# Kernel tuning notes

Measured on AMD Instinct MI355X. Metric: run time of the kernel, lower is better.

Reference implementation:

```python
import jax, jax.numpy as jnp
import numpy as np
from math import sqrt

N_HEADS = 16

def setup_inputs() -> dict:
    key = jax.random.key(0)
    ks = jax.random.split(key, 6)
    B, T, C = 4, 2048, 1024
    s = 0.02
    return {
        "X": jax.random.normal(ks[0], (B, T, C), jnp.float32),
        "Wq": jax.random.normal(ks[1], (C, C), jnp.float32) * s,
        "Wk": jax.random.normal(ks[2], (C, C), jnp.float32) * s,
        "Wv": jax.random.normal(ks[3], (C, C), jnp.float32) * s,
        "Wo": jax.random.normal(ks[4], (C, C), jnp.float32) * s,
        "bo": jnp.zeros((C,), jnp.float32),
    }

def reference(X, Wq, Wk, Wv, Wo, bo):
    B, T, C = X.shape
    H = N_HEADS
    D = C // H
    scale = sqrt(C / H)  # == sqrt(D)
    # Linear layers (torch Linear: y = x @ W.T), split into heads: [B,H,T,D]
    Q = (X @ Wq.T).reshape(B, T, H, D).transpose(0, 2, 1, 3)
    K = (X @ Wk.T).reshape(B, T, H, D).transpose(0, 2, 1, 3)
    V = (X @ Wv.T).reshape(B, T, H, D).transpose(0, 2, 1, 3)
    A = jnp.einsum("bhtd,bhsd->bhts", Q, K) / scale  # [B,H,T,T]
    causal = jnp.tril(jnp.ones((T, T), dtype=bool))
    A = jnp.where(causal, A, -jnp.inf)
    A = jax.nn.softmax(A, axis=-1)
    Y = jnp.einsum("bhts,bhsd->bhtd", A, V)  # [B,H,T,D]
    Y = Y.transpose(0, 2, 1, 3).reshape(B, T, C)
    return Y @ Wo.T + bo
```

## Files before the change

### kernel.cpp

```cpp
#include <hip/hip_runtime.h>
#include <hip/hip_bf16.h>
#include <stdint.h>


typedef unsigned short u16;
typedef __attribute__((ext_vector_type(8))) __bf16 bf16x8;
typedef __attribute__((ext_vector_type(4))) float  f32x4;
typedef __attribute__((ext_vector_type(4))) unsigned short u16x4;
typedef __attribute__((ext_vector_type(8))) unsigned short u16x8;
typedef __attribute__((ext_vector_type(4))) short s16x4;

#define B_  4
#define T_  2048
#define C_  1024
#define H_  16
#define D_  64
#define BT_ (B_ * T_)

#define Q_SCALE 0.1803368801111204f

__device__ __forceinline__ u16 f32_to_bf16(float f) {
    unsigned int u = __float_as_uint(f);
    unsigned int r = (u + 0x7FFFu + ((u >> 16) & 1u)) >> 16;
    return (u16)r;
}

__device__ __forceinline__ unsigned int pk_bf16(float a, float b) {
    float2 f2; f2.x = a; f2.y = b;
    __hip_bfloat162 h = __float22bfloat162_rn(f2);
    return *(unsigned int*)&h;
}

__device__ __forceinline__ void async16(const void* g, void* lds) {
    __builtin_amdgcn_global_load_lds(
        (const __attribute__((address_space(1))) void*)g,
        (__attribute__((address_space(3))) void*)lds, 16, 0, 0);
}

__global__ void cast_bf16_kernel(const float* __restrict__ in, u16* __restrict__ out, int n4) {
    int i = blockIdx.x * 256 + threadIdx.x;
    if (i >= n4) return;
    float4 v = ((const float4*)in)[i];
    u16x4 o;
    o[0] = f32_to_bf16(v.x); o[1] = f32_to_bf16(v.y);
    o[2] = f32_to_bf16(v.z); o[3] = f32_to_bf16(v.w);
    ((u16x4*)out)[i] = o;
}

__global__ void cast_w4_kernel(const float* __restrict__ w0, const float* __restrict__ w1,
                               const float* __restrict__ w2, const float* __restrict__ w3,
                               u16* __restrict__ o0, u16* __restrict__ o1,
                               u16* __restrict__ o2, u16* __restrict__ o3) {
    int which = blockIdx.y;
    const float* in = (which == 0) ? w0 : (which == 1) ? w1 : (which == 2) ? w2 : w3;
    u16* out = (which == 0) ? o0 : (which == 1) ? o1 : (which == 2) ? o2 : o3;
    int i = blockIdx.x * 256 + threadIdx.x;
    float4 v = ((const float4*)in)[i];
    u16x4 o;
    o[0] = f32_to_bf16(v.x); o[1] = f32_to_bf16(v.y);
    o[2] = f32_to_bf16(v.z); o[3] = f32_to_bf16(v.w);
    ((u16x4*)out)[i] = o;
}

__global__ __launch_bounds__(256, 2) void qkv_gemm(
    const u16* __restrict__ Xb,
    const u16* __restrict__ Wqb, const u16* __restrict__ Wkb, const u16* __restrict__ Wvb,
    u16* __restrict__ Qb, u16* __restrict__ Kb, u16* __restrict__ Vtb)
{
    __shared__ u16 Xs[8192];
    __shared__ u16 Wqs[8192], Wks[8192], Wvs[8192];

    int id = blockIdx.x;
    int xcd = id & 7;
    int local = id >> 3;
    int tt = xcd * 8 + (local & 7);
    int ct = local >> 3;
    int m0 = tt * 128, n0 = ct * 128;

    int tid = threadIdx.x, lane = tid & 63, w = tid >> 6;
    int quad = lane >> 4, l15 = lane & 15;
    int wm = w >> 1, wn = w & 1;

    int c0 = tid, c1 = tid + 256;
    int row0 = c0 >> 2, row1 = c1 >> 2;
    int gc0 = (((c0 & 3) - (row0 >> 1)) & 3) * 8;
    int gc1 = (((c1 & 3) - (row1 >> 1)) & 3) * 8;
    int ldsb0 = (w * 64) * 16;
    int ldsb1 = (256 + w * 64) * 16;

    const u16* xp0 = Xb  + (size_t)(m0 + row0) * C_ + gc0;
    const u16* xp1 = Xb  + (size_t)(m0 + row1) * C_ + gc1;
    const u16* wq0 = Wqb + (size_t)(n0 + row0) * C_ + gc0;
    const u16* wq1 = Wqb + (size_t)(n0 + row1) * C_ + gc1;
    const u16* wk0 = Wkb + (size_t)(n0 + row0) * C_ + gc0;
    const u16* wk1 = Wkb + (size_t)(n0 + row1) * C_ + gc1;
    const u16* wv0 = Wvb + (size_t)(n0 + row0) * C_ + gc0;
    const u16* wv1 = Wvb + (size_t)(n0 + row1) * C_ + gc1;

    int aoff[4], boff[4];
#pragma unroll
    for (int i = 0; i < 4; ++i) {
        int rA = wm * 64 + i * 16 + l15;
        aoff[i] = (rA * 32 + (((rA >> 1) + quad) & 3) * 8) * 2;
        int rB = wn * 64 + i * 16 + l15;
        boff[i] = (rB * 32 + (((rB >> 1) + quad) & 3) * 8) * 2;
    }

    f32x4 aq[4][4], ak[4][4], av[4][4];
    const f32x4 z4 = {0.f, 0.f, 0.f, 0.f};
#pragma unroll
    for (int i = 0; i < 4; ++i)
#pragma unroll
        for (int j = 0; j < 4; ++j) { aq[i][j] = z4; ak[i][j] = z4; av[i][j] = z4; }

    async16(xp0, (char*)Xs  + ldsb0); async16(xp1, (char*)Xs  + ldsb1);
    async16(wq0, (char*)Wqs + ldsb0); async16(wq1, (char*)Wqs + ldsb1);
    async16(wk0, (char*)Wks + ldsb0); async16(wk1, (char*)Wks + ldsb1);
    async16(wv0, (char*)Wvs + ldsb0); async16(wv1, (char*)Wvs + ldsb1);
    xp0 += 32; xp1 += 32; wq0 += 32; wq1 += 32;
    wk0 += 32; wk1 += 32; wv0 += 32; wv1 += 32;

    auto body = [&](int kt, int cur, int nxt) {
        __syncthreads();
        if (kt + 1 < 32) {
            async16(xp0, (char*)Xs  + nxt + ldsb0); async16(xp1, (char*)Xs  + nxt + ldsb1);
            async16(wq0, (char*)Wqs + nxt + ldsb0); async16(wq1, (char*)Wqs + nxt + ldsb1);
            async16(wk0, (char*)Wks + nxt + ldsb0); async16(wk1, (char*)Wks + nxt + ldsb1);
            async16(wv0, (char*)Wvs + nxt + ldsb0); async16(wv1, (char*)Wvs + nxt + ldsb1);
        }
        xp0 += 32; xp1 += 32; wq0 += 32; wq1 += 32;
        wk0 += 32; wk1 += 32; wv0 += 32; wv1 += 32;

        bf16x8 xa[4];
#pragma unroll
        for (int i = 0; i < 4; ++i)
            xa[i] = *(const bf16x8*)((const char*)Xs + cur + aoff[i]);

        bf16x8 bb[4];
#pragma unroll
        for (int j = 0; j < 4; ++j)
            bb[j] = *(const bf16x8*)((const char*)Wqs + cur + boff[j]);
#pragma unroll
        for (int j = 0; j < 4; ++j)
#pragma unroll
            for (int i = 0; i < 4; ++i)
                aq[j][i] = __builtin_amdgcn_mfma_f32_16x16x32_bf16(bb[j], xa[i], aq[j][i], 0, 0, 0);

#pragma unroll
        for (int j = 0; j < 4; ++j)
            bb[j] = *(const bf16x8*)((const char*)Wks + cur + boff[j]);
#pragma unroll
        for (int j = 0; j < 4; ++j)
#pragma unroll
            for (int i = 0; i < 4; ++i)
                ak[j][i] = __builtin_amdgcn_mfma_f32_16x16x32_bf16(bb[j], xa[i], ak[j][i], 0, 0, 0);

#pragma unroll
        for (int j = 0; j < 4; ++j)
            bb[j] = *(const bf16x8*)((const char*)Wvs + cur + boff[j]);
#pragma unroll
        for (int i = 0; i < 4; ++i)
#pragma unroll
            for (int j = 0; j < 4; ++j)
                av[i][j] = __builtin_amdgcn_mfma_f32_16x16x32_bf16(xa[i], bb[j], av[i][j], 0, 0, 0);
    };

    for (int kt = 0; kt < 32; kt += 2) {
        body(kt,     0,    8192);
        body(kt + 1, 8192, 0);
    }

#pragma unroll
    for (int j = 0; j < 4; ++j) {
        int ch0 = n0 + wn * 64 + j * 16 + quad * 4;
#pragma unroll
        for (int i = 0; i < 4; ++i) {
            int t = m0 + wm * 64 + i * 16 + l15;
            u16x4 vq, vk;
#pragma unroll
            for (int r = 0; r < 4; ++r) {
                vq[r] = f32_to_bf16(aq[j][i][r] * Q_SCALE);
                vk[r] = f32_to_bf16(ak[j][i][r]);
            }
            *(u16x4*)&Qb[(size_t)t * C_ + ch0] = vq;
            *(u16x4*)&Kb[(size_t)t * C_ + ch0] = vk;
        }
    }
#pragma unroll
    for (int i = 0; i < 4; ++i) {
        int t0 = m0 + wm * 64 + i * 16 + quad * 4;
        int bb_ = t0 >> 11, tloc = t0 & (T_ - 1);
#pragma unroll
        for (int j = 0; j < 4; ++j) {
            int col = n0 + wn * 64 + j * 16 + l15;
            int h = col >> 6, d = col & 63;
            u16x4 v;
#pragma unroll
            for (int r = 0; r < 4; ++r) v[r] = f32_to_bf16(av[i][j][r]);
            *(u16x4*)&Vtb[(((bb_ * H_ + h) * D_ + d) * T_) + tloc] = v;
        }
    }
}

__device__ __forceinline__ void gemm_core_128_db(
    const u16* __restrict__ A, const u16* __restrict__ B,
    u16* As, u16* Bs, int m0, int n0, f32x4 (&acc)[4][4])
{
    const int K = C_;
    const int KT = K / 32;
    int tid  = threadIdx.x;
    int lane = tid & 63, w = tid >> 6;
    int quad = lane >> 4, l15 = lane & 15;
    int wm = w >> 1, wn = w & 1;

    int c0 = tid, c1 = tid + 256;
    int row0 = c0 >> 2, row1 = c1 >> 2;
    int gc0 = (((c0 & 3) - (row0 >> 1)) & 3) * 8;
    int gc1 = (((c1 & 3) - (row1 >> 1)) & 3) * 8;
    int ldsb0 = (w * 64) * 16;
    int ldsb1 = (256 + w * 64) * 16;

    const u16* ApA = A + (size_t)(m0 + row0) * K + gc0;
    const u16* ApB = A + (size_t)(m0 + row1) * K + gc1;
    const u16* BpA = B + (size_t)(n0 + row0) * K + gc0;
    const u16* BpB = B + (size_t)(n0 + row1) * K + gc1;

    char* As0 = (char*)As; char* As1 = (char*)As + 8192;
    char* Bs0 = (char*)Bs; char* Bs1 = (char*)Bs + 8192;

    int aoff[4], boff[4];
#pragma unroll
    for (int i = 0; i < 4; ++i) {
        int rA = wm * 64 + i * 16 + l15;
        aoff[i] = (rA * 32 + (((rA >> 1) + quad) & 3) * 8) * 2;
        int rB = wn * 64 + i * 16 + l15;
        boff[i] = (rB * 32 + (((rB >> 1) + quad) & 3) * 8) * 2;
    }

    async16(ApA, As0 + ldsb0); async16(ApB, As0 + ldsb1);
    async16(BpA, Bs0 + ldsb0); async16(BpB, Bs0 + ldsb1);
    ApA += 32; ApB += 32; BpA += 32; BpB += 32;

    auto body = [&](int kt, const char* Ac, const char* Bc, char* Apf, char* Bpf) {
        __syncthreads();
        if (kt + 1 < KT) {
            async16(ApA, Apf + ldsb0); async16(ApB, Apf + ldsb1);
            async16(BpA, Bpf + ldsb0); async16(BpB, Bpf + ldsb1);
        }
        ApA += 32; ApB += 32; BpA += 32; BpB += 32;

        bf16x8 a[4], b[4];
#pragma unroll
        for (int i = 0; i < 4; ++i) {
            a[i] = *(const bf16x8*)(Ac + aoff[i]);
            b[i] = *(const bf16x8*)(Bc + boff[i]);
        }
#pragma unroll
        for (int i = 0; i < 4; ++i)
#pragma unroll
            for (int j = 0; j < 4; ++j)
                acc[i][j] = __builtin_amdgcn_mfma_f32_16x16x32_bf16(a[i], b[j], acc[i][j], 0, 0, 0);
    };

    for (int kt = 0; kt < KT; kt += 2) {
        body(kt,     As0, Bs0, As1, Bs1);
        body(kt + 1, As1, Bs1, As0, Bs0);
    }
}

__global__ __launch_bounds__(256) void attn_kernel(
    const u16* __restrict__ Qb, const u16* __restrict__ Kb,
    const u16* __restrict__ Vtb, u16* __restrict__ Yb)
{
    __shared__ u16 SMA[16384];
    u16* Ks0 = SMA;
    u16* Ks1 = SMA + 4096;
    u16* Vs0 = SMA + 8192;
    u16* Vs1 = SMA + 12288;

    int id = blockIdx.x;
    int kk = id >> 8;
    int cc = id & 255;
    int jj = cc >> 6;
    int bh = cc & 63;
    int qt = (kk == 0) ? jj : (kk == 1) ? (15 - jj) : (kk == 2) ? (jj + 4) : (11 - jj);

    int tid = threadIdx.x, lane = tid & 63, w = tid >> 6;
    int quad = lane >> 4, l15 = lane & 15;
    int qbase = qt * 128;
    int b = bh >> 4, h = bh & 15;

    bf16x8 qf[2][2];
    {
        const u16* q0 = Qb + ((size_t)(b * T_ + qbase + w * 32 + l15)) * C_ + h * 64;
        qf[0][0] = *(const bf16x8*)(q0 + quad * 8);
        qf[0][1] = *(const bf16x8*)(q0 + 32 + quad * 8);
        const u16* q1 = q0 + 16 * C_;
        qf[1][0] = *(const bf16x8*)(q1 + quad * 8);
        qf[1][1] = *(const bf16x8*)(q1 + 32 + quad * 8);
    }

    int koff0[4], koff1[4], voff[4][4];
#pragma unroll
    for (int sblk = 0; sblk < 4; ++sblk) {
        int sr = sblk * 16 + l15;
        koff0[sblk] = (sr * 64 + ((quad + sr) & 7) * 8) * 2;
        koff1[sblk] = (sr * 64 + ((4 + quad + sr) & 7) * 8) * 2;
    }
#pragma unroll
    for (int n = 0; n < 4; ++n)
#pragma unroll
        for (int sblk = 0; sblk < 4; ++sblk) {
            int dr = n * 16 + l15;
            voff[n][sblk] = (dr * 64 + ((sblk * 2 + (quad >> 1) + dr) & 7) * 8 + (quad & 1) * 4) * 2;
        }

    float l_part[2] = {0.f, 0.f};
    f32x4 o_acc[2][4];
    const f32x4 z4 = {0.f, 0.f, 0.f, 0.f};
#pragma unroll
    for (int c = 0; c < 2; ++c)
#pragma unroll
        for (int n = 0; n < 4; ++n) o_acc[c][n] = z4;

    int cA = tid, cB = tid + 256;
    int sA = cA >> 3, sB = cB >> 3;
    int offA = (((cA & 7) - sA) & 7) * 8;
    int offB = (((cB & 7) - sB) & 7) * 8;
    const u16* Kbase = Kb + (size_t)(b * T_) * C_ + h * 64;
    const u16* Vbase = Vtb + (size_t)bh * D_ * T_;
    int ldsb0 = (w * 64) * 16, ldsb1 = (256 + w * 64) * 16;

    const int nst = 2 * qt + 2;

    const u16* kgpA = Kbase + (size_t)sA * C_ + offA;
    const u16* kgpB = Kbase + (size_t)sB * C_ + offB;
    const u16* vgpA = Vbase + sA * T_ + offA;
    const u16* vgpB = Vbase + sB * T_ + offB;

    async16(kgpA, (char*)Ks0 + ldsb0);
    async16(kgpB, (char*)Ks0 + ldsb1);
    async16(vgpA, (char*)Vs0 + ldsb0);
    async16(vgpB, (char*)Vs0 + ldsb1);
    kgpA += 64 * C_; kgpB += 64 * C_; vgpA += 64; vgpB += 64;

    auto tile_body = [&](int st, const u16* K_, const u16* V_, char* Kpf, char* Vpf) {
        __syncthreads();
        if (st + 1 < nst) {
            async16(kgpA, Kpf + ldsb0);
            async16(kgpB, Kpf + ldsb1);
            async16(vgpA, Vpf + ldsb0);
            async16(vgpB, Vpf + ldsb1);
        }
        kgpA += 64 * C_; kgpB += 64 * C_; vgpA += 64; vgpB += 64;

        f32x4 sv[2][4];
#pragma unroll
        for (int sblk = 0; sblk < 4; ++sblk) {
            bf16x8 k0 = *(const bf16x8*)((const char*)K_ + koff0[sblk]);
            bf16x8 k1 = *(const bf16x8*)((const char*)K_ + koff1[sblk]);
#pragma unroll
            for (int c = 0; c < 2; ++c) {
                f32x4 t0 = __builtin_amdgcn_mfma_f32_16x16x32_bf16(k0, qf[c][0], z4, 0, 0, 0);
                sv[c][sblk] = __builtin_amdgcn_mfma_f32_16x16x32_bf16(k1, qf[c][1], t0, 0, 0, 0);
            }
        }

        if (st >= 2 * qt) {
            int sb0 = st * 64 - qbase;
#pragma unroll
            for (int c = 0; c < 2; ++c) {
                int tl = w * 32 + c * 16 + l15;
#pragma unroll
                for (int sblk = 0; sblk < 4; ++sblk)
#pragma unroll
                    for (int r = 0; r < 4; ++r)
                        if (sb0 + sblk * 16 + quad * 4 + r > tl) sv[c][sblk][r] = -1e30f;
            }
        }

        s16x4 pfrag[2][4];
#pragma unroll
        for (int c = 0; c < 2; ++c) {
            f32x4 s4 = z4;
#pragma unroll
            for (int sblk = 0; sblk < 4; ++sblk) {
#pragma unroll
                for (int r = 0; r < 4; ++r)
                    sv[c][sblk][r] = __builtin_amdgcn_exp2f(sv[c][sblk][r]);
                s4 += sv[c][sblk];
                uint2 pk;
                pk.x = pk_bf16(sv[c][sblk][0], sv[c][sblk][1]);
                pk.y = pk_bf16(sv[c][sblk][2], sv[c][sblk][3]);
                pfrag[c][sblk] = *(s16x4*)&pk;
            }
            l_part[c] += (s4[0] + s4[1]) + (s4[2] + s4[3]);
        }

#pragma unroll
        for (int n = 0; n < 4; ++n)
#pragma unroll
            for (int sblk = 0; sblk < 4; ++sblk) {
                s16x4 va = *(const s16x4*)((const char*)V_ + voff[n][sblk]);
#pragma unroll
                for (int c = 0; c < 2; ++c)
                    o_acc[c][n] = __builtin_amdgcn_mfma_f32_16x16x16bf16_1k(va, pfrag[c][sblk], o_acc[c][n], 0, 0, 0);
            }
    };

    for (int st = 0; st < nst; st += 2) {
        tile_body(st,     Ks0, Vs0, (char*)Ks1, (char*)Vs1);
        tile_body(st + 1, Ks1, Vs1, (char*)Ks0, (char*)Vs0);
    }

    __syncthreads();
    u16* PW = SMA + w * 2304;
#pragma unroll
    for (int c = 0; c < 2; ++c) {
        float l = l_part[c];
        l += __shfl_xor(l, 16, 64);
        l += __shfl_xor(l, 32, 64);
        float inv = 1.0f / l;
#pragma unroll
        for (int n = 0; n < 4; ++n) {
            u16x4 v;
            uint2 pk;
            pk.x = pk_bf16(o_acc[c][n][0] * inv, o_acc[c][n][1] * inv);
            pk.y = pk_bf16(o_acc[c][n][2] * inv, o_acc[c][n][3] * inv);
            v = *(u16x4*)&pk;
            *(u16x4*)&PW[(c * 16 + l15) * 72 + n * 16 + quad * 4] = v;
        }
    }
    asm volatile("s_waitcnt lgkmcnt(0)" ::: "memory");
#pragma unroll
    for (int st = 0; st < 4; ++st) {
        int tr = st * 8 + (lane >> 3);
        int d8 = (lane & 7) * 8;
        u16x8 v = *(u16x8*)&PW[tr * 72 + d8];
        *(u16x8*)&Yb[(size_t)(b * T_ + qbase + w * 32 + tr) * C_ + h * 64 + d8] = v;
    }
}

__global__ __launch_bounds__(256, 4) void proj_gemm(
    const u16* __restrict__ Yb, const u16* __restrict__ Wob,
    const float* __restrict__ bo, float* __restrict__ out)
{
    __shared__ u16 SM[17408];
    u16* As = SM;
    u16* Bs = SM + 8192;

    int id = blockIdx.x;
    int xcd = id & 7;
    int local = id >> 3;
    int by = xcd * 8 + (local & 7);
    int bx = local >> 3;
    int m0 = bx * 128, n0 = by * 128;

    f32x4 acc[4][4];
    const f32x4 z4 = {0.f, 0.f, 0.f, 0.f};
#pragma unroll
    for (int i = 0; i < 4; ++i)
#pragma unroll
        for (int j = 0; j < 4; ++j) acc[i][j] = z4;

    gemm_core_128_db(Wob, Yb, As, Bs, m0, n0, acc);

    int lane = threadIdx.x & 63, w = threadIdx.x >> 6;
    int quad = lane >> 4, l15 = lane & 15;
    int wm = w >> 1, wn = w & 1;

    float* LF = (float*)SM;
    __syncthreads();
#pragma unroll
    for (int hh = 0; hh < 2; ++hh) {
        if (wm == hh) {
#pragma unroll
            for (int i = 0; i < 4; ++i) {
                int chl = i * 16 + quad * 4;
#pragma unroll
                for (int j = 0; j < 4; ++j) {
                    int tl = wn * 64 + j * 16 + l15;
                    *(f32x4*)&LF[tl * 68 + chl] = acc[i][j];
                }
            }
        }
        __syncthreads();
        f32x4 b4 = *(const f32x4*)&bo[m0 + hh * 64 + (lane & 15) * 4];
#pragma unroll
        for (int st = 0; st < 8; ++st) {
            int tl = w * 32 + st * 4 + (lane >> 4);
            int ch4 = (lane & 15) * 4;
            f32x4 v = *(f32x4*)&LF[tl * 68 + ch4];
            v += b4;
            *(f32x4*)&out[(size_t)(n0 + tl) * C_ + m0 + hh * 64 + ch4] = v;
        }
        if (hh == 0) __syncthreads();
    }
}

extern "C" void kernel_launch(void* const* d_in, const int* in_sizes, int n_in,
                              void* d_out, int out_size, void* d_ws, size_t ws_size,
                              hipStream_t stream) {
    const float* X  = (const float*)d_in[0];
    const float* Wq = (const float*)d_in[1];
    const float* Wk = (const float*)d_in[2];
    const float* Wv = (const float*)d_in[3];
    const float* Wo = (const float*)d_in[4];
    const float* bo = (const float*)d_in[5];

    char* ws = (char*)d_ws;
    u16* Xb  = (u16*)(ws);
    u16* Wqb = (u16*)(ws + (16u << 20));
    u16* Wkb = (u16*)(ws + (18u << 20));
    u16* Wvb = (u16*)(ws + (20u << 20));
    u16* Wob = (u16*)(ws + (22u << 20));
    u16* Qb  = (u16*)(ws + (24u << 20));
    u16* Kb  = (u16*)(ws + (40u << 20));
    u16* Vtb = (u16*)(ws + (56u << 20));
    u16* Yb  = (u16*)(ws + (72u << 20));

    cast_bf16_kernel<<<(BT_ * C_ / 4) / 256, 256, 0, stream>>>(X, Xb, BT_ * C_ / 4);
    cast_w4_kernel<<<dim3((C_ * C_ / 4) / 256, 4), 256, 0, stream>>>(
        Wq, Wk, Wv, Wo, Wqb, Wkb, Wvb, Wob);

    qkv_gemm<<<dim3(512), 256, 0, stream>>>(Xb, Wqb, Wkb, Wvb, Qb, Kb, Vtb);
    attn_kernel<<<dim3((T_ / 128) * B_ * H_), 256, 0, stream>>>(Qb, Kb, Vtb, Yb);
    proj_gemm<<<dim3(8 * 64), 256, 0, stream>>>(Yb, Wob, bo, (float*)d_out);
}
```

Before: 264.1 us.

## Pair causal query tiles per block and compute row sums via MFMA

The attention kernel now launches 512 blocks, each processing two query tiles (jj and 15-jj) in sequence, so every block does the same amount of causal work instead of relying on block-order scheduling to balance tiles. The softmax denominator is accumulated with an extra MFMA against a vector of ones rather than with scalar adds and cross-lane shuffles. In exchange, per-block serial work doubles and there are fewer blocks to hide latency, and the extra MFMA per fragment adds matrix-unit work. The sum now uses bf16-rounded probabilities, which slightly changes numerics.

```diff
diff --git a/kernel.cpp b/kernel.cpp
--- a/kernel.cpp
+++ b/kernel.cpp
@@ -279,26 +279,12 @@
     u16* Vs1 = SMA + 12288;
 
     int id = blockIdx.x;
-    int kk = id >> 8;
-    int cc = id & 255;
-    int jj = cc >> 6;
-    int bh = cc & 63;
-    int qt = (kk == 0) ? jj : (kk == 1) ? (15 - jj) : (kk == 2) ? (jj + 4) : (11 - jj);
+    int bh = id & 63;
+    int jj = id >> 6;
 
     int tid = threadIdx.x, lane = tid & 63, w = tid >> 6;
     int quad = lane >> 4, l15 = lane & 15;
-    int qbase = qt * 128;
     int b = bh >> 4, h = bh & 15;
-
-    bf16x8 qf[2][2];
-    {
-        const u16* q0 = Qb + ((size_t)(b * T_ + qbase + w * 32 + l15)) * C_ + h * 64;
-        qf[0][0] = *(const bf16x8*)(q0 + quad * 8);
-        qf[0][1] = *(const bf16x8*)(q0 + 32 + quad * 8);
-        const u16* q1 = q0 + 16 * C_;
-        qf[1][0] = *(const bf16x8*)(q1 + quad * 8);
-        qf[1][1] = *(const bf16x8*)(q1 + 32 + quad * 8);
-    }
 
     int koff0[4], koff1[4], voff[4][4];
 #pragma unroll
@@ -314,14 +300,6 @@
             int dr = n * 16 + l15;
             voff[n][sblk] = (dr * 64 + ((sblk * 2 + (quad >> 1) + dr) & 7) * 8 + (quad & 1) * 4) * 2;
         }
-
-    float l_part[2] = {0.f, 0.f};
-    f32x4 o_acc[2][4];
-    const f32x4 z4 = {0.f, 0.f, 0.f, 0.f};
-#pragma unroll
-    for (int c = 0; c < 2; ++c)
-#pragma unroll
-        for (int n = 0; n < 4; ++n) o_acc[c][n] = z4;
 
     int cA = tid, cB = tid + 256;
     int sA = cA >> 3, sB = cB >> 3;
@@ -331,113 +309,139 @@
     const u16* Vbase = Vtb + (size_t)bh * D_ * T_;
     int ldsb0 = (w * 64) * 16, ldsb1 = (256 + w * 64) * 16;
 
-    const int nst = 2 * qt + 2;
-
-    const u16* kgpA = Kbase + (size_t)sA * C_ + offA;
-    const u16* kgpB = Kbase + (size_t)sB * C_ + offB;
-    const u16* vgpA = Vbase + sA * T_ + offA;
-    const u16* vgpB = Vbase + sB * T_ + offB;
-
-    async16(kgpA, (char*)Ks0 + ldsb0);
-    async16(kgpB, (char*)Ks0 + ldsb1);
-    async16(vgpA, (char*)Vs0 + ldsb0);
-    async16(vgpB, (char*)Vs0 + ldsb1);
-    kgpA += 64 * C_; kgpB += 64 * C_; vgpA += 64; vgpB += 64;
-
-    auto tile_body = [&](int st, const u16* K_, const u16* V_, char* Kpf, char* Vpf) {
+    const s16x4 ones = { (short)0x3F80, (short)0x3F80, (short)0x3F80, (short)0x3F80 };
+    const f32x4 z4 = {0.f, 0.f, 0.f, 0.f};
+
+    int qts[2] = { jj, 15 - jj };
+
+    for (int pass = 0; pass < 2; ++pass) {
+        int qt = qts[pass];
+        int qbase = qt * 128;
+
+        if (pass) __syncthreads();
+
+        bf16x8 qf[2][2];
+        {
+            const u16* q0 = Qb + ((size_t)(b * T_ + qbase + w * 32 + l15)) * C_ + h * 64;
+            qf[0][0] = *(const bf16x8*)(q0 + quad * 8);
+            qf[0][1] = *(const bf16x8*)(q0 + 32 + quad * 8);
+            const u16* q1 = q0 + 16 * C_;
+            qf[1][0] = *(const bf16x8*)(q1 + quad * 8);
+            qf[1][1] = *(const bf16x8*)(q1 + 32 + quad * 8);
+        }
+
+        f32x4 o_acc[2][4];
+        f32x4 l_acc[2];
+#pragma unroll
+        for (int c = 0; c < 2; ++c) {
+            l_acc[c] = z4;
+#pragma unroll
+            for (int n = 0; n < 4; ++n) o_acc[c][n] = z4;
+        }
+
+        const int nst = 2 * qt + 2;
+
+        const u16* kgpA = Kbase + (size_t)sA * C_ + offA;
+        const u16* kgpB = Kbase + (size_t)sB * C_ + offB;
+        const u16* vgpA = Vbase + sA * T_ + offA;
+        const u16* vgpB = Vbase + sB * T_ + offB;
+
+        async16(kgpA, (char*)Ks0 + ldsb0);
+        async16(kgpB, (char*)Ks0 + ldsb1);
+        async16(vgpA, (char*)Vs0 + ldsb0);
+        async16(vgpB, (char*)Vs0 + ldsb1);
+        kgpA += 64 * C_; kgpB += 64 * C_; vgpA += 64; vgpB += 64;
+
+        auto tile_body = [&](int st, const u16* K_, const u16* V_, char* Kpf, char* Vpf) {
+            __syncthreads();
+            if (st + 1 < nst) {
+                async16(kgpA, Kpf + ldsb0);
+                async16(kgpB, Kpf + ldsb1);
+                async16(vgpA, Vpf + ldsb0);
+                async16(vgpB, Vpf + ldsb1);
+            }
+            kgpA += 64 * C_; kgpB += 64 * C_; vgpA += 64; vgpB += 64;
+
+            f32x4 sv[2][4];
+#pragma unroll
+            for (int sblk = 0; sblk < 4; ++sblk) {
+                bf16x8 k0 = *(const bf16x8*)((const char*)K_ + koff0[sblk]);
+                bf16x8 k1 = *(const bf16x8*)((const char*)K_ + koff1[sblk]);
+#pragma unroll
+                for (int c = 0; c < 2; ++c) {
+                    f32x4 t0 = __builtin_amdgcn_mfma_f32_16x16x32_bf16(k0, qf[c][0], z4, 0, 0, 0);
+                    sv[c][sblk] = __builtin_amdgcn_mfma_f32_16x16x32_bf16(k1, qf[c][1], t0, 0, 0, 0);
+                }
+            }
+
+            if (st >= 2 * qt) {
+                int sb0 = st * 64 - qbase;
+#pragma unroll
+                for (int c = 0; c < 2; ++c) {
+                    int tl = w * 32 + c * 16 + l15;
+#pragma unroll
+                    for (int sblk = 0; sblk < 4; ++sblk)
+#pragma unroll
+                        for (int r = 0; r < 4; ++r)
+                            if (sb0 + sblk * 16 + quad * 4 + r > tl) sv[c][sblk][r] = -1e30f;
+                }
+            }
+
+            s16x4 pfrag[2][4];
+#pragma unroll
+            for (int c = 0; c < 2; ++c) {
+#pragma unroll
+                for (int sblk = 0; sblk < 4; ++sblk) {
+#pragma unroll
+                    for (int r = 0; r < 4; ++r)
+                        sv[c][sblk][r] = __builtin_amdgcn_exp2f(sv[c][sblk][r]);
+                    uint2 pk;
+                    pk.x = pk_bf16(sv[c][sblk][0], sv[c][sblk][1]);
+                    pk.y = pk_bf16(sv[c][sblk][2], sv[c][sblk][3]);
+                    pfrag[c][sblk] = *(s16x4*)&pk;
+                    l_acc[c] = __builtin_amdgcn_mfma_f32_16x16x16bf16_1k(ones, pfrag[c][sblk], l_acc[c], 0, 0, 0);
+                }
+            }
+
+#pragma unroll
+            for (int n = 0; n < 4; ++n)
+#pragma unroll
+                for (int sblk = 0; sblk < 4; ++sblk) {
+                    s16x4 va = *(const s16x4*)((const char*)V_ + voff[n][sblk]);
+#pragma unroll
+                    for (int c = 0; c < 2; ++c)
+                        o_acc[c][n] = __builtin_amdgcn_mfma_f32_16x16x16bf16_1k(va, pfrag[c][sblk], o_acc[c][n], 0, 0, 0);
+                }
+        };
+
+        for (int st = 0; st < nst; st += 2) {
+            tile_body(st,     Ks0, Vs0, (char*)Ks1, (char*)Vs1);
+            tile_body(st + 1, Ks1, Vs1, (char*)Ks0, (char*)Vs0);
+        }
+
         __syncthreads();
-        if (st + 1 < nst) {
-            async16(kgpA, Kpf + ldsb0);
-            async16(kgpB, Kpf + ldsb1);
-            async16(vgpA, Vpf + ldsb0);
-            async16(vgpB, Vpf + ldsb1);
-        }
-        kgpA += 64 * C_; kgpB += 64 * C_; vgpA += 64; vgpB += 64;
-
-        f32x4 sv[2][4];
-#pragma unroll
-        for (int sblk = 0; sblk < 4; ++sblk) {
-            bf16x8 k0 = *(const bf16x8*)((const char*)K_ + koff0[sblk]);
-            bf16x8 k1 = *(const bf16x8*)((const char*)K_ + koff1[sblk]);
-#pragma unroll
-            for (int c = 0; c < 2; ++c) {
-                f32x4 t0 = __builtin_amdgcn_mfma_f32_16x16x32_bf16(k0, qf[c][0], z4, 0, 0, 0);
-                sv[c][sblk] = __builtin_amdgcn_mfma_f32_16x16x32_bf16(k1, qf[c][1], t0, 0, 0, 0);
-            }
-        }
-
-        if (st >= 2 * qt) {
-            int sb0 = st * 64 - qbase;
-#pragma unroll
-            for (int c = 0; c < 2; ++c) {
-                int tl = w * 32 + c * 16 + l15;
-#pragma unroll
-                for (int sblk = 0; sblk < 4; ++sblk)
-#pragma unroll
-                    for (int r = 0; r < 4; ++r)
-                        if (sb0 + sblk * 16 + quad * 4 + r > tl) sv[c][sblk][r] = -1e30f;
-            }
-        }
-
-        s16x4 pfrag[2][4];
+        u16* PW = SMA + w * 2304;
 #pragma unroll
         for (int c = 0; c < 2; ++c) {
-            f32x4 s4 = z4;
-#pragma unroll
-            for (int sblk = 0; sblk < 4; ++sblk) {
-#pragma unroll
-                for (int r = 0; r < 4; ++r)
-                    sv[c][sblk][r] = __builtin_amdgcn_exp2f(sv[c][sblk][r]);
-                s4 += sv[c][sblk];
+            float inv = 1.0f / l_acc[c][0];
+#pragma unroll
+            for (int n = 0; n < 4; ++n) {
+                u16x4 v;
                 uint2 pk;
-                pk.x = pk_bf16(sv[c][sblk][0], sv[c][sblk][1]);
-                pk.y = pk_bf16(sv[c][sblk][2], sv[c][sblk][3]);
-                pfrag[c][sblk] = *(s16x4*)&pk;
-            }
-            l_part[c] += (s4[0] + s4[1]) + (s4[2] + s4[3]);
-        }
-
-#pragma unroll
-        for (int n = 0; n < 4; ++n)
-#pragma unroll
-            for (int sblk = 0; sblk < 4; ++sblk) {
-                s16x4 va = *(const s16x4*)((const char*)V_ + voff[n][sblk]);
-#pragma unroll
-                for (int c = 0; c < 2; ++c)
-                    o_acc[c][n] = __builtin_amdgcn_mfma_f32_16x16x16bf16_1k(va, pfrag[c][sblk], o_acc[c][n], 0, 0, 0);
-            }
-    };
-
-    for (int st = 0; st < nst; st += 2) {
-        tile_body(st,     Ks0, Vs0, (char*)Ks1, (char*)Vs1);
-        tile_body(st + 1, Ks1, Vs1, (char*)Ks0, (char*)Vs0);
-    }
-
-    __syncthreads();
-    u16* PW = SMA + w * 2304;
-#pragma unroll
-    for (int c = 0; c < 2; ++c) {
-        float l = l_part[c];
-        l += __shfl_xor(l, 16, 64);
-        l += __shfl_xor(l, 32, 64);
-        float inv = 1.0f / l;
-#pragma unroll
-        for (int n = 0; n < 4; ++n) {
-            u16x4 v;
-            uint2 pk;
-            pk.x = pk_bf16(o_acc[c][n][0] * inv, o_acc[c][n][1] * inv);
-            pk.y = pk_bf16(o_acc[c][n][2] * inv, o_acc[c][n][3] * inv);
-            v = *(u16x4*)&pk;
-            *(u16x4*)&PW[(c * 16 + l15) * 72 + n * 16 + quad * 4] = v;
-        }
-    }
-    asm volatile("s_waitcnt lgkmcnt(0)" ::: "memory");
-#pragma unroll
-    for (int st = 0; st < 4; ++st) {
-        int tr = st * 8 + (lane >> 3);
-        int d8 = (lane & 7) * 8;
-        u16x8 v = *(u16x8*)&PW[tr * 72 + d8];
-        *(u16x8*)&Yb[(size_t)(b * T_ + qbase + w * 32 + tr) * C_ + h * 64 + d8] = v;
+                pk.x = pk_bf16(o_acc[c][n][0] * inv, o_acc[c][n][1] * inv);
+                pk.y = pk_bf16(o_acc[c][n][2] * inv, o_acc[c][n][3] * inv);
+                v = *(u16x4*)&pk;
+                *(u16x4*)&PW[(c * 16 + l15) * 72 + n * 16 + quad * 4] = v;
+            }
+        }
+        asm volatile("s_waitcnt lgkmcnt(0)" ::: "memory");
+#pragma unroll
+        for (int st = 0; st < 4; ++st) {
+            int tr = st * 8 + (lane >> 3);
+            int d8 = (lane & 7) * 8;
+            u16x8 v = *(u16x8*)&PW[tr * 72 + d8];
+            *(u16x8*)&Yb[(size_t)(b * T_ + qbase + w * 32 + tr) * C_ + h * 64 + d8] = v;
+        }
     }
 }
 
@@ -524,6 +528,6 @@
         Wq, Wk, Wv, Wo, Wqb, Wkb, Wvb, Wob);
 
     qkv_gemm<<<dim3(512), 256, 0, stream>>>(Xb, Wqb, Wkb, Wvb, Qb, Kb, Vtb);
-    attn_kernel<<<dim3((T_ / 128) * B_ * H_), 256, 0, stream>>>(Qb, Kb, Vtb, Yb);
+    attn_kernel<<<dim3(512), 256, 0, stream>>>(Qb, Kb, Vtb, Yb);
     proj_gemm<<<dim3(8 * 64), 256, 0, stream>>>(Yb, Wob, bo, (float*)d_out);
 }
```

Measured after the change: 262.8 us. No clear change (-0.5%).
